# Optimization experiments

Hardware: AMD Instinct MI355X
Metric: run time of the kernel (lower is better)

## Reference

```python
import jax, jax.numpy as jnp
import numpy as np
from jax import lax

AROUND_R = 0.1  # init default


def bilinear_sample(img, grid):
    """img: [B,C,H,W]; grid: [B,A,N,2] in [-1,1]; returns [B,C,A,N].
    Matches F.grid_sample(mode='bilinear', padding_mode='zeros', align_corners=False)."""
    B, C, H, W = img.shape
    x = (grid[..., 0] + 1.0) * (W / 2) - 0.5  # unnormalize, align_corners=False
    y = (grid[..., 1] + 1.0) * (H / 2) - 0.5
    x0 = jnp.floor(x)
    y0 = jnp.floor(y)
    wx1 = x - x0
    wy1 = y - y0
    wx0 = 1.0 - wx1
    wy0 = 1.0 - wy1
    imgf = img.reshape(B, C, H * W)
    A, N = grid.shape[1], grid.shape[2]

    def gather(ix, iy):
        valid = (ix >= 0) & (ix <= W - 1) & (iy >= 0) & (iy <= H - 1)
        idx = (jnp.clip(iy, 0, H - 1) * W + jnp.clip(ix, 0, W - 1)).astype(jnp.int32)
        vals = jax.vmap(lambda im, ii: im[:, ii])(imgf, idx.reshape(B, A * N))  # [B,C,A*N]
        return vals.reshape(B, C, A, N) * valid[:, None].astype(img.dtype)

    v00 = gather(x0, y0)
    v10 = gather(x0 + 1, y0)
    v01 = gather(x0, y0 + 1)
    v11 = gather(x0 + 1, y0 + 1)
    return (v00 * (wx0 * wy0)[:, None] + v10 * (wx1 * wy0)[:, None]
            + v01 * (wx0 * wy1)[:, None] + v11 * (wx1 * wy1)[:, None])


def soft_align(x1, points_feature, points, pos_emb_2d, around_offsets):
    # --- torch.no_grad() block: grid and replicated features are detached ---
    grid = points[:, None, :, :]                                  # [B,1,N,2]
    around = (around_offsets * 2.0 - 0.5) * 2.0 * AROUND_R        # [B,A,N,2]
    g = lax.stop_gradient(jnp.clip(grid + around, -1.0, 1.0))     # [B,A,N,2]
    rep = lax.stop_gradient(points_feature)                       # [B,N,C]
    rep = rep.transpose(0, 2, 1)[:, :, None, :]                   # [B,C,1,N]
    # --- differentiable part ---
    emb = bilinear_sample(pos_emb_2d, g)                          # [B,C,A,N]
    feat = bilinear_sample(x1, g)                                 # [B,C,A,N]
    eps = 1e-8  # torch cosine_similarity default
    dot = jnp.sum(rep * feat, axis=1)                             # [B,A,N]
    na = jnp.maximum(jnp.sqrt(jnp.sum(rep * rep, axis=1)), eps)   # [B,1,N]
    nb = jnp.maximum(jnp.sqrt(jnp.sum(feat * feat, axis=1)), eps)
    sim = dot / (na * nb)                                         # [B,A,N]
    w = jax.nn.softmax(sim, axis=1)                               # softmax over A
    weighted = jnp.sum(emb * w[:, None], axis=2)                  # [B,C,N]
    return points_feature + weighted.transpose(0, 2, 1)           # [B,N,C]


def setup_inputs() -> dict:
    key = jax.random.key(0)
    k1, k2, k3, k4, k5 = jax.random.split(key, 5)
    B, C, H, W, N, A = 4, 256, 128, 128, 4096, 5
    x1 = jax.random.normal(k1, (B, C, H, W), jnp.float32)
    points_feature = jax.random.normal(k2, (B, N, C), jnp.float32)
    points = jax.random.uniform(k3, (B, N, 2), jnp.float32, -1.0, 1.0)
    pos_emb_2d = jax.random.normal(k4, (B, C, H, W), jnp.float32)
    around_offsets = jax.random.uniform(k5, (B, A, N, 2), jnp.float32)  # torch.rand
    return {"x1": x1, "points_feature": points_feature, "points": points,
            "pos_emb_2d": pos_emb_2d, "around_offsets": around_offsets}


def reference(x1, points_feature, points, pos_emb_2d, around_offsets):
    return soft_align(x1, points_feature, points, pos_emb_2d, around_offsets)
```

## Files before the change

### kernel.cpp

```cpp
#include <hip/hip_runtime.h>
#include <hip/hip_bf16.h>
#include <math.h>

constexpr int B = 4, C = 256, H = 128, W = 128, N = 4096, A = 5;
constexpr int HWs = H * W;
constexpr float AROUND_R = 0.1f;
constexpr int NP = B * N;

__device__ __forceinline__ float ulo(unsigned u) {
    union { unsigned i; float f; } x; x.i = u << 16; return x.f;
}
__device__ __forceinline__ float uhi(unsigned u) {
    union { unsigned i; float f; } x; x.i = u & 0xffff0000u; return x.f;
}
__device__ __forceinline__ float red64(float v) {
    #pragma unroll
    for (int off = 32; off > 0; off >>= 1)
        v += __shfl_xor(v, off);
    return v;
}

#if __has_builtin(__builtin_amdgcn_cvt_pk_f32_fp8) && __has_builtin(__builtin_amdgcn_cvt_pk_fp8_f32)
#define FP8_HW 1
#endif

__device__ __forceinline__ unsigned enc_fp8_sw(float x) {
    unsigned s = (__float_as_uint(x) >> 31) << 7;
    float ax = fminf(fabsf(x), 448.0f);
    if (!(ax >= 0x1p-10f)) return s;
    int e = (int)((__float_as_uint(ax) >> 23) & 0xff) - 127;
    e = e < -6 ? -6 : e;
    float q = rintf(ldexpf(ax, 3 - e));
    int iq = (int)q;
    if (iq >= 16) { iq = 8; e += 1; }
    unsigned enc = (iq >= 8) ? (((unsigned)(e + 7) << 3) | (unsigned)(iq - 8))
                             : (unsigned)iq;
    return s | enc;
}
__device__ __forceinline__ float dec_fp8_sw(unsigned u) {
    unsigned s = u >> 7, E = (u >> 3) & 0xf, M = u & 7;
    float v = E ? __uint_as_float(((E + 120u) << 23) | (M << 20)) : (float)M * 0x1p-9f;
    return s ? -v : v;
}

__device__ __forceinline__ unsigned pack4_fp8(float a0, float a1, float a2, float a3) {
#ifdef FP8_HW
    int w = __builtin_amdgcn_cvt_pk_fp8_f32(a0, a1, 0, false);
    w = __builtin_amdgcn_cvt_pk_fp8_f32(a2, a3, w, true);
    return (unsigned)w;
#else
    return enc_fp8_sw(a0) | (enc_fp8_sw(a1) << 8) | (enc_fp8_sw(a2) << 16) | (enc_fp8_sw(a3) << 24);
#endif
}
__device__ __forceinline__ void fp8x4_to_f32(unsigned u, float* f) {
#ifdef FP8_HW
    auto lo = __builtin_amdgcn_cvt_pk_f32_fp8((int)u, false);
    auto hi = __builtin_amdgcn_cvt_pk_f32_fp8((int)u, true);
    f[0] = lo[0]; f[1] = lo[1]; f[2] = hi[0]; f[3] = hi[1];
#else
    f[0] = dec_fp8_sw(u & 0xff); f[1] = dec_fp8_sw((u >> 8) & 0xff);
    f[2] = dec_fp8_sw((u >> 16) & 0xff); f[3] = dec_fp8_sw(u >> 24);
#endif
}

__global__ __launch_bounds__(256) void transpose_x1_fp8(const float* __restrict__ in,
                                                        unsigned* __restrict__ outw) {
    constexpr int TILE = 32;
    __shared__ float t[TILE][C + 1];
    const int tilesPerB = HWs / TILE;
    int bx = blockIdx.x;
    int b  = bx / tilesPerB;
    int hw0 = (bx % tilesPerB) * TILE;
    int tid  = threadIdx.x;
    int hw_l = tid & 31;
    int cg   = tid >> 5;

    const float* src = in + (size_t)b * C * HWs;
    #pragma unroll
    for (int ci = 0; ci < C / 8; ++ci) {
        int c = ci * 8 + cg;
        t[hw_l][c] = src[(size_t)c * HWs + hw0 + hw_l];
    }
    __syncthreads();
    unsigned* dst = outw + ((size_t)b * HWs + hw0) * (C / 4);
    int dq = tid & 63, pg = tid >> 6;
    #pragma unroll
    for (int it = 0; it < 8; ++it) {
        int pix = it * 4 + pg;
        float a0 = t[pix][dq * 4 + 0], a1 = t[pix][dq * 4 + 1];
        float a2 = t[pix][dq * 4 + 2], a3 = t[pix][dq * 4 + 3];
        dst[(size_t)pix * (C / 4) + dq] = pack4_fp8(a0, a1, a2, a3);
    }
}

__global__ __launch_bounds__(256) void transpose_pe_bf16(const float* __restrict__ in,
                                                         __hip_bfloat16* __restrict__ out) {
    constexpr int TILE = 32;
    __shared__ float t[TILE][C + 1];
    const int tilesPerB = HWs / TILE;
    int bx = blockIdx.x;
    int b  = bx / tilesPerB;
    int hw0 = (bx % tilesPerB) * TILE;
    int tid  = threadIdx.x;
    int hw_l = tid & 31;
    int cg   = tid >> 5;

    const float* src = in + (size_t)b * C * HWs;
    #pragma unroll
    for (int ci = 0; ci < C / 8; ++ci) {
        int c = ci * 8 + cg;
        t[hw_l][c] = src[(size_t)c * HWs + hw0 + hw_l];
    }
    __syncthreads();
    __hip_bfloat16* dst = out + ((size_t)b * HWs + hw0) * C;
    #pragma unroll
    for (int hwi = 0; hwi < TILE; ++hwi) {
        dst[(size_t)hwi * C + tid] = __float2bfloat16(t[hwi][tid]);
    }
}

__global__ __launch_bounds__(256) void soft_align_v5(
    const unsigned char* __restrict__ x1f8,
    const ushort* __restrict__ pebf,
    const float* __restrict__ pf,
    const float* __restrict__ pts,
    const float* __restrict__ ao,
    float* __restrict__ out)
{
    int tid = threadIdx.x, lane = tid & 63, wave = tid >> 6;
    int p = blockIdx.x * 4 + wave;
    int b = p >> 12, n = p & (N - 1);
    size_t pn = (size_t)p;

    float gx0 = pts[pn * 2 + 0];
    float gy0 = pts[pn * 2 + 1];
    float2 aov[A];
    #pragma unroll
    for (int a = 0; a < A; ++a)
        aov[a] = *reinterpret_cast<const float2*>(ao + (((size_t)b * A + a) * N + n) * 2);

    float4 rep4 = *reinterpret_cast<const float4*>(pf + pn * C + lane * 4);

    int   sidx[A][4];
    float swgt[A][4];
    #pragma unroll
    for (int a = 0; a < A; ++a) {
        float gx = fminf(fmaxf(gx0 + (aov[a].x * 2.0f - 0.5f) * (2.0f * AROUND_R), -1.0f), 1.0f);
        float gy = fminf(fmaxf(gy0 + (aov[a].y * 2.0f - 0.5f) * (2.0f * AROUND_R), -1.0f), 1.0f);
        float x = (gx + 1.0f) * (W * 0.5f) - 0.5f;
        float y = (gy + 1.0f) * (H * 0.5f) - 0.5f;
        float fx0 = floorf(x), fy0 = floorf(y);
        float wx1 = x - fx0, wy1 = y - fy0;
        float wx0 = 1.0f - wx1, wy0 = 1.0f - wy1;
        int ix0 = (int)fx0, iy0 = (int)fy0, ix1 = ix0 + 1, iy1 = iy0 + 1;
        bool vx0 = (ix0 >= 0) & (ix0 < W), vx1 = (ix1 >= 0) & (ix1 < W);
        bool vy0 = (iy0 >= 0) & (iy0 < H), vy1 = (iy1 >= 0) & (iy1 < H);
        int cx0 = min(max(ix0, 0), W - 1), cx1 = min(max(ix1, 0), W - 1);
        int cy0 = min(max(iy0, 0), H - 1), cy1 = min(max(iy1, 0), H - 1);
        int id0 = cy0 * W + cx0, id1 = cy0 * W + cx1;
        int id2 = cy1 * W + cx0, id3 = cy1 * W + cx1;
        sidx[a][0] = __builtin_amdgcn_readfirstlane(id0);
        sidx[a][1] = __builtin_amdgcn_readfirstlane(id1);
        sidx[a][2] = __builtin_amdgcn_readfirstlane(id2);
        sidx[a][3] = __builtin_amdgcn_readfirstlane(id3);
        swgt[a][0] = (vx0 && vy0) ? wx0 * wy0 : 0.0f;
        swgt[a][1] = (vx1 && vy0) ? wx1 * wy0 : 0.0f;
        swgt[a][2] = (vx0 && vy1) ? wx0 * wy1 : 0.0f;
        swgt[a][3] = (vx1 && vy1) ? wx1 * wy1 : 0.0f;
    }

    const unsigned char* xb = x1f8 + (size_t)b * HWs * C;
    const ushort*        pb = pebf + (size_t)b * HWs * C;
    unsigned xv[A][4];
    #pragma unroll
    for (int a = 0; a < A; ++a)
        #pragma unroll
        for (int k = 0; k < 4; ++k)
            xv[a][k] = *reinterpret_cast<const unsigned*>(xb + (size_t)sidx[a][k] * C + lane * 4);
    uint2 pv[A][4];
    #pragma unroll
    for (int a = 0; a < A; ++a)
        #pragma unroll
        for (int k = 0; k < 4; ++k)
            pv[a][k] = *reinterpret_cast<const uint2*>(pb + (size_t)sidx[a][k] * C + lane * 4);

    float na2 = rep4.x * rep4.x + rep4.y * rep4.y + rep4.z * rep4.z + rep4.w * rep4.w;
    float dt[A], nb[A];
    #pragma unroll
    for (int a = 0; a < A; ++a) {
        float f0 = 0.f, f1 = 0.f, f2 = 0.f, f3 = 0.f;
        #pragma unroll
        for (int k = 0; k < 4; ++k) {
            float w = swgt[a][k];
            float c4[4];
            fp8x4_to_f32(xv[a][k], c4);
            f0 += w * c4[0]; f1 += w * c4[1]; f2 += w * c4[2]; f3 += w * c4[3];
        }
        dt[a] = rep4.x * f0 + rep4.y * f1 + rep4.z * f2 + rep4.w * f3;
        nb[a] = f0 * f0 + f1 * f1 + f2 * f2 + f3 * f3;
    }

    na2 = red64(na2);
    #pragma unroll
    for (int a = 0; a < A; ++a) dt[a] = red64(dt[a]);
    #pragma unroll
    for (int a = 0; a < A; ++a) nb[a] = red64(nb[a]);
    float na = fmaxf(sqrtf(na2), 1e-8f);

    float sim[A];
    #pragma unroll
    for (int a = 0; a < A; ++a)
        sim[a] = dt[a] / (na * fmaxf(sqrtf(nb[a]), 1e-8f));

    float m = sim[0];
    #pragma unroll
    for (int a = 1; a < A; ++a) m = fmaxf(m, sim[a]);
    float e[A], s = 0.f;
    #pragma unroll
    for (int a = 0; a < A; ++a) { e[a] = __expf(sim[a] - m); s += e[a]; }
    float inv = 1.0f / s;

    float o0 = rep4.x, o1 = rep4.y, o2 = rep4.z, o3 = rep4.w;
    #pragma unroll
    for (int a = 0; a < A; ++a) {
        float wa = e[a] * inv;
        #pragma unroll
        for (int k = 0; k < 4; ++k) {
            float c = wa * swgt[a][k];
            unsigned u0 = pv[a][k].x, u1 = pv[a][k].y;
            o0 += c * ulo(u0); o1 += c * uhi(u0);
            o2 += c * ulo(u1); o3 += c * uhi(u1);
        }
    }
    *reinterpret_cast<float4*>(out + pn * C + lane * 4) = make_float4(o0, o1, o2, o3);
}

extern "C" void kernel_launch(void* const* d_in, const int* in_sizes, int n_in,
                              void* d_out, int out_size, void* d_ws, size_t ws_size,
                              hipStream_t stream) {
    const float* x1  = (const float*)d_in[0];
    const float* pf  = (const float*)d_in[1];
    const float* pts = (const float*)d_in[2];
    const float* pe  = (const float*)d_in[3];
    const float* ao  = (const float*)d_in[4];
    float* out = (float*)d_out;

    unsigned* x1f8w = (unsigned*)d_ws;
    __hip_bfloat16* pebf = (__hip_bfloat16*)((char*)d_ws + (size_t)B * HWs * C);

    int tblocks = B * (HWs / 32);
    transpose_x1_fp8 <<<tblocks, 256, 0, stream>>>(x1, x1f8w);
    transpose_pe_bf16<<<tblocks, 256, 0, stream>>>(pe, pebf);
    soft_align_v5<<<NP / 4, 256, 0, stream>>>((const unsigned char*)x1f8w,
                                              (const ushort*)pebf, pf, pts, ao, out);
}
```

Measured before the change: 66.12 us.

## Interleave fp8 x1 and bf16 pos-emb per pixel into one padded record

Measured after the change: 97.96 us. 48.1% more time.

```diff
diff --git a/kernel.cpp b/kernel.cpp
--- a/kernel.cpp
+++ b/kernel.cpp
@@ -6,12 +6,19 @@
 constexpr int HWs = H * W;
 constexpr float AROUND_R = 0.1f;
 constexpr int NP = B * N;
+constexpr int PIXB = 1024;
 
 __device__ __forceinline__ float ulo(unsigned u) {
     union { unsigned i; float f; } x; x.i = u << 16; return x.f;
 }
 __device__ __forceinline__ float uhi(unsigned u) {
     union { unsigned i; float f; } x; x.i = u & 0xffff0000u; return x.f;
+}
+__device__ __forceinline__ unsigned pk2bf(float a, float b) {
+    unsigned ua = __float_as_uint(a), ub = __float_as_uint(b);
+    ua = (ua + 0x7fffu + ((ua >> 16) & 1u)) >> 16;
+    ub = (ub + 0x7fffu + ((ub >> 16) & 1u)) & 0xffff0000u;
+    return ua | ub;
 }
 __device__ __forceinline__ float red64(float v) {
     #pragma unroll
@@ -42,7 +49,6 @@
     float v = E ? __uint_as_float(((E + 120u) << 23) | (M << 20)) : (float)M * 0x1p-9f;
     return s ? -v : v;
 }
-
 __device__ __forceinline__ unsigned pack4_fp8(float a0, float a1, float a2, float a3) {
 #ifdef FP8_HW
     int w = __builtin_amdgcn_cvt_pk_fp8_f32(a0, a1, 0, false);
@@ -64,7 +70,7 @@
 }
 
 __global__ __launch_bounds__(256) void transpose_x1_fp8(const float* __restrict__ in,
-                                                        unsigned* __restrict__ outw) {
+                                                        char* __restrict__ imgs) {
     constexpr int TILE = 32;
     __shared__ float t[TILE][C + 1];
     const int tilesPerB = HWs / TILE;
@@ -82,19 +88,20 @@
         t[hw_l][c] = src[(size_t)c * HWs + hw0 + hw_l];
     }
     __syncthreads();
-    unsigned* dst = outw + ((size_t)b * HWs + hw0) * (C / 4);
+    char* base = imgs + ((size_t)b * HWs + hw0) * PIXB;
     int dq = tid & 63, pg = tid >> 6;
     #pragma unroll
     for (int it = 0; it < 8; ++it) {
         int pix = it * 4 + pg;
         float a0 = t[pix][dq * 4 + 0], a1 = t[pix][dq * 4 + 1];
         float a2 = t[pix][dq * 4 + 2], a3 = t[pix][dq * 4 + 3];
-        dst[(size_t)pix * (C / 4) + dq] = pack4_fp8(a0, a1, a2, a3);
+        *reinterpret_cast<unsigned*>(base + (size_t)pix * PIXB + 16 * dq + 8) =
+            pack4_fp8(a0, a1, a2, a3);
     }
 }
 
 __global__ __launch_bounds__(256) void transpose_pe_bf16(const float* __restrict__ in,
-                                                         __hip_bfloat16* __restrict__ out) {
+                                                         char* __restrict__ imgs) {
     constexpr int TILE = 32;
     __shared__ float t[TILE][C + 1];
     const int tilesPerB = HWs / TILE;
@@ -112,16 +119,20 @@
         t[hw_l][c] = src[(size_t)c * HWs + hw0 + hw_l];
     }
     __syncthreads();
-    __hip_bfloat16* dst = out + ((size_t)b * HWs + hw0) * C;
-    #pragma unroll
-    for (int hwi = 0; hwi < TILE; ++hwi) {
-        dst[(size_t)hwi * C + tid] = __float2bfloat16(t[hwi][tid]);
-    }
-}
-
-__global__ __launch_bounds__(256) void soft_align_v5(
-    const unsigned char* __restrict__ x1f8,
-    const ushort* __restrict__ pebf,
+    char* base = imgs + ((size_t)b * HWs + hw0) * PIXB;
+    int dq = tid & 63, pg = tid >> 6;
+    #pragma unroll
+    for (int it = 0; it < 8; ++it) {
+        int pix = it * 4 + pg;
+        float a0 = t[pix][dq * 4 + 0], a1 = t[pix][dq * 4 + 1];
+        float a2 = t[pix][dq * 4 + 2], a3 = t[pix][dq * 4 + 3];
+        uint2 w = make_uint2(pk2bf(a0, a1), pk2bf(a2, a3));
+        *reinterpret_cast<uint2*>(base + (size_t)pix * PIXB + 16 * dq) = w;
+    }
+}
+
+__global__ __launch_bounds__(256) void soft_align_v6(
+    const char* __restrict__ imgs,
     const float* __restrict__ pf,
     const float* __restrict__ pts,
     const float* __restrict__ ao,
@@ -132,8 +143,7 @@
     int b = p >> 12, n = p & (N - 1);
     size_t pn = (size_t)p;
 
-    float gx0 = pts[pn * 2 + 0];
-    float gy0 = pts[pn * 2 + 1];
+    float2 g0 = *reinterpret_cast<const float2*>(pts + pn * 2);
     float2 aov[A];
     #pragma unroll
     for (int a = 0; a < A; ++a)
@@ -145,8 +155,8 @@
     float swgt[A][4];
     #pragma unroll
     for (int a = 0; a < A; ++a) {
-        float gx = fminf(fmaxf(gx0 + (aov[a].x * 2.0f - 0.5f) * (2.0f * AROUND_R), -1.0f), 1.0f);
-        float gy = fminf(fmaxf(gy0 + (aov[a].y * 2.0f - 0.5f) * (2.0f * AROUND_R), -1.0f), 1.0f);
+        float gx = fminf(fmaxf(g0.x + (aov[a].x * 2.0f - 0.5f) * (2.0f * AROUND_R), -1.0f), 1.0f);
+        float gy = fminf(fmaxf(g0.y + (aov[a].y * 2.0f - 0.5f) * (2.0f * AROUND_R), -1.0f), 1.0f);
         float x = (gx + 1.0f) * (W * 0.5f) - 0.5f;
         float y = (gy + 1.0f) * (H * 0.5f) - 0.5f;
         float fx0 = floorf(x), fy0 = floorf(y);
@@ -157,47 +167,43 @@
         bool vy0 = (iy0 >= 0) & (iy0 < H), vy1 = (iy1 >= 0) & (iy1 < H);
         int cx0 = min(max(ix0, 0), W - 1), cx1 = min(max(ix1, 0), W - 1);
         int cy0 = min(max(iy0, 0), H - 1), cy1 = min(max(iy1, 0), H - 1);
-        int id0 = cy0 * W + cx0, id1 = cy0 * W + cx1;
-        int id2 = cy1 * W + cx0, id3 = cy1 * W + cx1;
-        sidx[a][0] = __builtin_amdgcn_readfirstlane(id0);
-        sidx[a][1] = __builtin_amdgcn_readfirstlane(id1);
-        sidx[a][2] = __builtin_amdgcn_readfirstlane(id2);
-        sidx[a][3] = __builtin_amdgcn_readfirstlane(id3);
+        sidx[a][0] = __builtin_amdgcn_readfirstlane(cy0 * W + cx0);
+        sidx[a][1] = __builtin_amdgcn_readfirstlane(cy0 * W + cx1);
+        sidx[a][2] = __builtin_amdgcn_readfirstlane(cy1 * W + cx0);
+        sidx[a][3] = __builtin_amdgcn_readfirstlane(cy1 * W + cx1);
         swgt[a][0] = (vx0 && vy0) ? wx0 * wy0 : 0.0f;
         swgt[a][1] = (vx1 && vy0) ? wx1 * wy0 : 0.0f;
         swgt[a][2] = (vx0 && vy1) ? wx0 * wy1 : 0.0f;
         swgt[a][3] = (vx1 && vy1) ? wx1 * wy1 : 0.0f;
     }
 
-    const unsigned char* xb = x1f8 + (size_t)b * HWs * C;
-    const ushort*        pb = pebf + (size_t)b * HWs * C;
-    unsigned xv[A][4];
+    const char* ib = imgs + (size_t)b * HWs * PIXB + 16 * lane;
+    uint4 v[A][4];
     #pragma unroll
     for (int a = 0; a < A; ++a)
         #pragma unroll
         for (int k = 0; k < 4; ++k)
-            xv[a][k] = *reinterpret_cast<const unsigned*>(xb + (size_t)sidx[a][k] * C + lane * 4);
-    uint2 pv[A][4];
-    #pragma unroll
-    for (int a = 0; a < A; ++a)
-        #pragma unroll
-        for (int k = 0; k < 4; ++k)
-            pv[a][k] = *reinterpret_cast<const uint2*>(pb + (size_t)sidx[a][k] * C + lane * 4);
+            v[a][k] = *reinterpret_cast<const uint4*>(ib + (size_t)sidx[a][k] * PIXB);
 
     float na2 = rep4.x * rep4.x + rep4.y * rep4.y + rep4.z * rep4.z + rep4.w * rep4.w;
-    float dt[A], nb[A];
+    float dt[A], nb[A], emb[A][4];
     #pragma unroll
     for (int a = 0; a < A; ++a) {
         float f0 = 0.f, f1 = 0.f, f2 = 0.f, f3 = 0.f;
+        float e0 = 0.f, e1 = 0.f, e2 = 0.f, e3 = 0.f;
         #pragma unroll
         for (int k = 0; k < 4; ++k) {
             float w = swgt[a][k];
+            unsigned pl = v[a][k].x, ph = v[a][k].y, xw = v[a][k].z;
             float c4[4];
-            fp8x4_to_f32(xv[a][k], c4);
+            fp8x4_to_f32(xw, c4);
             f0 += w * c4[0]; f1 += w * c4[1]; f2 += w * c4[2]; f3 += w * c4[3];
+            e0 += w * ulo(pl); e1 += w * uhi(pl);
+            e2 += w * ulo(ph); e3 += w * uhi(ph);
         }
         dt[a] = rep4.x * f0 + rep4.y * f1 + rep4.z * f2 + rep4.w * f3;
         nb[a] = f0 * f0 + f1 * f1 + f2 * f2 + f3 * f3;
+        emb[a][0] = e0; emb[a][1] = e1; emb[a][2] = e2; emb[a][3] = e3;
     }
 
     na2 = red64(na2);
@@ -224,13 +230,8 @@
     #pragma unroll
     for (int a = 0; a < A; ++a) {
         float wa = e[a] * inv;
-        #pragma unroll
-        for (int k = 0; k < 4; ++k) {
-            float c = wa * swgt[a][k];
-            unsigned u0 = pv[a][k].x, u1 = pv[a][k].y;
-            o0 += c * ulo(u0); o1 += c * uhi(u0);
-            o2 += c * ulo(u1); o3 += c * uhi(u1);
-        }
+        o0 += wa * emb[a][0]; o1 += wa * emb[a][1];
+        o2 += wa * emb[a][2]; o3 += wa * emb[a][3];
     }
     *reinterpret_cast<float4*>(out + pn * C + lane * 4) = make_float4(o0, o1, o2, o3);
 }
@@ -245,12 +246,10 @@
     const float* ao  = (const float*)d_in[4];
     float* out = (float*)d_out;
 
-    unsigned* x1f8w = (unsigned*)d_ws;
-    __hip_bfloat16* pebf = (__hip_bfloat16*)((char*)d_ws + (size_t)B * HWs * C);
+    char* imgs = (char*)d_ws;
 
     int tblocks = B * (HWs / 32);
-    transpose_x1_fp8 <<<tblocks, 256, 0, stream>>>(x1, x1f8w);
-    transpose_pe_bf16<<<tblocks, 256, 0, stream>>>(pe, pebf);
-    soft_align_v5<<<NP / 4, 256, 0, stream>>>((const unsigned char*)x1f8w,
-                                              (const ushort*)pebf, pf, pts, ao, out);
-}
+    transpose_x1_fp8 <<<tblocks, 256, 0, stream>>>(x1, imgs);
+    transpose_pe_bf16<<<tblocks, 256, 0, stream>>>(pe, imgs);
+    soft_align_v6<<<NP / 4, 256, 0, stream>>>(imgs, pf, pts, ao, out);
+}
```

## Overlap pos-emb transpose with similarity pass by splitting into three kernels

Applied to the files above, without the earlier changes.

Result: slower. 71.47 us (+8.1%).

```diff
diff --git a/kernel.cpp b/kernel.cpp
--- a/kernel.cpp
+++ b/kernel.cpp
@@ -42,7 +42,6 @@
     float v = E ? __uint_as_float(((E + 120u) << 23) | (M << 20)) : (float)M * 0x1p-9f;
     return s ? -v : v;
 }
-
 __device__ __forceinline__ unsigned pack4_fp8(float a0, float a1, float a2, float a3) {
 #ifdef FP8_HW
     int w = __builtin_amdgcn_cvt_pk_fp8_f32(a0, a1, 0, false);
@@ -61,6 +60,28 @@
     f[0] = dec_fp8_sw(u & 0xff); f[1] = dec_fp8_sw((u >> 8) & 0xff);
     f[2] = dec_fp8_sw((u >> 16) & 0xff); f[3] = dec_fp8_sw(u >> 24);
 #endif
+}
+
+__device__ __forceinline__ void corner_math(float gx0, float gy0, float2 aov,
+                                            int* id, float* wg) {
+    float gx = fminf(fmaxf(gx0 + (aov.x * 2.0f - 0.5f) * (2.0f * AROUND_R), -1.0f), 1.0f);
+    float gy = fminf(fmaxf(gy0 + (aov.y * 2.0f - 0.5f) * (2.0f * AROUND_R), -1.0f), 1.0f);
+    float x = (gx + 1.0f) * (W * 0.5f) - 0.5f;
+    float y = (gy + 1.0f) * (H * 0.5f) - 0.5f;
+    float fx0 = floorf(x), fy0 = floorf(y);
+    float wx1 = x - fx0, wy1 = y - fy0;
+    float wx0 = 1.0f - wx1, wy0 = 1.0f - wy1;
+    int ix0 = (int)fx0, iy0 = (int)fy0, ix1 = ix0 + 1, iy1 = iy0 + 1;
+    bool vx0 = (ix0 >= 0) & (ix0 < W), vx1 = (ix1 >= 0) & (ix1 < W);
+    bool vy0 = (iy0 >= 0) & (iy0 < H), vy1 = (iy1 >= 0) & (iy1 < H);
+    int cx0 = min(max(ix0, 0), W - 1), cx1 = min(max(ix1, 0), W - 1);
+    int cy0 = min(max(iy0, 0), H - 1), cy1 = min(max(iy1, 0), H - 1);
+    id[0] = cy0 * W + cx0; id[1] = cy0 * W + cx1;
+    id[2] = cy1 * W + cx0; id[3] = cy1 * W + cx1;
+    wg[0] = (vx0 && vy0) ? wx0 * wy0 : 0.0f;
+    wg[1] = (vx1 && vy0) ? wx1 * wy0 : 0.0f;
+    wg[2] = (vx0 && vy1) ? wx0 * wy1 : 0.0f;
+    wg[3] = (vx1 && vy1) ? wx1 * wy1 : 0.0f;
 }
 
 __global__ __launch_bounds__(256) void transpose_x1_fp8(const float* __restrict__ in,
@@ -93,38 +114,124 @@
     }
 }
 
-__global__ __launch_bounds__(256) void transpose_pe_bf16(const float* __restrict__ in,
-                                                         __hip_bfloat16* __restrict__ out) {
-    constexpr int TILE = 32;
-    __shared__ float t[TILE][C + 1];
-    const int tilesPerB = HWs / TILE;
-    int bx = blockIdx.x;
-    int b  = bx / tilesPerB;
-    int hw0 = (bx % tilesPerB) * TILE;
-    int tid  = threadIdx.x;
-    int hw_l = tid & 31;
-    int cg   = tid >> 5;
-
-    const float* src = in + (size_t)b * C * HWs;
-    #pragma unroll
-    for (int ci = 0; ci < C / 8; ++ci) {
-        int c = ci * 8 + cg;
-        t[hw_l][c] = src[(size_t)c * HWs + hw0 + hw_l];
-    }
-    __syncthreads();
-    __hip_bfloat16* dst = out + ((size_t)b * HWs + hw0) * C;
-    #pragma unroll
-    for (int hwi = 0; hwi < TILE; ++hwi) {
-        dst[(size_t)hwi * C + tid] = __float2bfloat16(t[hwi][tid]);
-    }
-}
-
-__global__ __launch_bounds__(256) void soft_align_v5(
+__global__ __launch_bounds__(256) void k2_petrans_sim(
+    const float* __restrict__ pe,
+    __hip_bfloat16* __restrict__ pebf,
     const unsigned char* __restrict__ x1f8,
+    const float* __restrict__ pf,
+    const float* __restrict__ pts,
+    const float* __restrict__ ao,
+    float* __restrict__ wout)
+{
+    __shared__ float t[32][C + 1];
+    int bid = blockIdx.x;
+    int r = bid % 3, tb = bid / 3;
+    int tid = threadIdx.x;
+
+    if (r == 0) {
+        const int tilesPerB = HWs / 32;
+        int b  = tb / tilesPerB;
+        int hw0 = (tb % tilesPerB) * 32;
+        int hw_l = tid & 31, cg = tid >> 5;
+        const float* src = pe + (size_t)b * C * HWs;
+        #pragma unroll
+        for (int ci = 0; ci < C / 8; ++ci) {
+            int c = ci * 8 + cg;
+            t[hw_l][c] = src[(size_t)c * HWs + hw0 + hw_l];
+        }
+        __syncthreads();
+        __hip_bfloat16* dst = pebf + ((size_t)b * HWs + hw0) * C;
+        #pragma unroll
+        for (int hwi = 0; hwi < 32; ++hwi) {
+            dst[(size_t)hwi * C + tid] = __float2bfloat16(t[hwi][tid]);
+        }
+        return;
+    }
+
+    int sb = 2 * tb + (r - 1);
+    int lane = tid & 63, wave = tid >> 6;
+    int p = sb * 4 + wave;
+    int b = p >> 12, n = p & (N - 1);
+    size_t pn = (size_t)p;
+
+    float2 g0 = *reinterpret_cast<const float2*>(pts + pn * 2);
+    float2 aov[A];
+    #pragma unroll
+    for (int a = 0; a < A; ++a)
+        aov[a] = *reinterpret_cast<const float2*>(ao + (((size_t)b * A + a) * N + n) * 2);
+
+    float4 rep4 = *reinterpret_cast<const float4*>(pf + pn * C + lane * 4);
+
+    int   sidx[A][4];
+    float swgt[A][4];
+    #pragma unroll
+    for (int a = 0; a < A; ++a) {
+        int id[4]; float wg[4];
+        corner_math(g0.x, g0.y, aov[a], id, wg);
+        #pragma unroll
+        for (int k = 0; k < 4; ++k) {
+            sidx[a][k] = __builtin_amdgcn_readfirstlane(id[k]);
+            swgt[a][k] = wg[k];
+        }
+    }
+
+    const unsigned char* xb = x1f8 + (size_t)b * HWs * C;
+    unsigned xv[A][4];
+    #pragma unroll
+    for (int a = 0; a < A; ++a)
+        #pragma unroll
+        for (int k = 0; k < 4; ++k)
+            xv[a][k] = *reinterpret_cast<const unsigned*>(xb + (size_t)sidx[a][k] * C + lane * 4);
+
+    float na2 = rep4.x * rep4.x + rep4.y * rep4.y + rep4.z * rep4.z + rep4.w * rep4.w;
+    float dt[A], nb[A];
+    #pragma unroll
+    for (int a = 0; a < A; ++a) {
+        float f0 = 0.f, f1 = 0.f, f2 = 0.f, f3 = 0.f;
+        #pragma unroll
+        for (int k = 0; k < 4; ++k) {
+            float w = swgt[a][k];
+            float c4[4];
+            fp8x4_to_f32(xv[a][k], c4);
+            f0 += w * c4[0]; f1 += w * c4[1]; f2 += w * c4[2]; f3 += w * c4[3];
+        }
+        dt[a] = rep4.x * f0 + rep4.y * f1 + rep4.z * f2 + rep4.w * f3;
+        nb[a] = f0 * f0 + f1 * f1 + f2 * f2 + f3 * f3;
+    }
+
+    na2 = red64(na2);
+    #pragma unroll
+    for (int a = 0; a < A; ++a) dt[a] = red64(dt[a]);
+    #pragma unroll
+    for (int a = 0; a < A; ++a) nb[a] = red64(nb[a]);
+    float na = fmaxf(sqrtf(na2), 1e-8f);
+
+    float sim[A];
+    #pragma unroll
+    for (int a = 0; a < A; ++a)
+        sim[a] = dt[a] / (na * fmaxf(sqrtf(nb[a]), 1e-8f));
+
+    float m = sim[0];
+    #pragma unroll
+    for (int a = 1; a < A; ++a) m = fmaxf(m, sim[a]);
+    float e[A], s = 0.f;
+    #pragma unroll
+    for (int a = 0; a < A; ++a) { e[a] = __expf(sim[a] - m); s += e[a]; }
+    float inv = 1.0f / s;
+
+    if (lane == 0) {
+        *reinterpret_cast<float4*>(wout + pn * 8) =
+            make_float4(e[0] * inv, e[1] * inv, e[2] * inv, e[3] * inv);
+        wout[pn * 8 + 4] = e[4] * inv;
+    }
+}
+
+__global__ __launch_bounds__(256) void k3_emb(
     const ushort* __restrict__ pebf,
     const float* __restrict__ pf,
     const float* __restrict__ pts,
     const float* __restrict__ ao,
+    const float* __restrict__ wsm,
     float* __restrict__ out)
 {
     int tid = threadIdx.x, lane = tid & 63, wave = tid >> 6;
@@ -132,51 +239,30 @@
     int b = p >> 12, n = p & (N - 1);
     size_t pn = (size_t)p;
 
-    float gx0 = pts[pn * 2 + 0];
-    float gy0 = pts[pn * 2 + 1];
+    float2 g0 = *reinterpret_cast<const float2*>(pts + pn * 2);
     float2 aov[A];
     #pragma unroll
     for (int a = 0; a < A; ++a)
         aov[a] = *reinterpret_cast<const float2*>(ao + (((size_t)b * A + a) * N + n) * 2);
 
-    float4 rep4 = *reinterpret_cast<const float4*>(pf + pn * C + lane * 4);
+    float4 w03 = *reinterpret_cast<const float4*>(wsm + pn * 8);
+    float  w4  = wsm[pn * 8 + 4];
+    float wa[A] = {w03.x, w03.y, w03.z, w03.w, w4};
 
     int   sidx[A][4];
-    float swgt[A][4];
+    float cwt[A][4];
     #pragma unroll
     for (int a = 0; a < A; ++a) {
-        float gx = fminf(fmaxf(gx0 + (aov[a].x * 2.0f - 0.5f) * (2.0f * AROUND_R), -1.0f), 1.0f);
-        float gy = fminf(fmaxf(gy0 + (aov[a].y * 2.0f - 0.5f) * (2.0f * AROUND_R), -1.0f), 1.0f);
-        float x = (gx + 1.0f) * (W * 0.5f) - 0.5f;
-        float y = (gy + 1.0f) * (H * 0.5f) - 0.5f;
-        float fx0 = floorf(x), fy0 = floorf(y);
-        float wx1 = x - fx0, wy1 = y - fy0;
-        float wx0 = 1.0f - wx1, wy0 = 1.0f - wy1;
-        int ix0 = (int)fx0, iy0 = (int)fy0, ix1 = ix0 + 1, iy1 = iy0 + 1;
-        bool vx0 = (ix0 >= 0) & (ix0 < W), vx1 = (ix1 >= 0) & (ix1 < W);
-        bool vy0 = (iy0 >= 0) & (iy0 < H), vy1 = (iy1 >= 0) & (iy1 < H);
-        int cx0 = min(max(ix0, 0), W - 1), cx1 = min(max(ix1, 0), W - 1);
-        int cy0 = min(max(iy0, 0), H - 1), cy1 = min(max(iy1, 0), H - 1);
-        int id0 = cy0 * W + cx0, id1 = cy0 * W + cx1;
-        int id2 = cy1 * W + cx0, id3 = cy1 * W + cx1;
-        sidx[a][0] = __builtin_amdgcn_readfirstlane(id0);
-        sidx[a][1] = __builtin_amdgcn_readfirstlane(id1);
-        sidx[a][2] = __builtin_amdgcn_readfirstlane(id2);
-        sidx[a][3] = __builtin_amdgcn_readfirstlane(id3);
-        swgt[a][0] = (vx0 && vy0) ? wx0 * wy0 : 0.0f;
-        swgt[a][1] = (vx1 && vy0) ? wx1 * wy0 : 0.0f;
-        swgt[a][2] = (vx0 && vy1) ? wx0 * wy1 : 0.0f;
-        swgt[a][3] = (vx1 && vy1) ? wx1 * wy1 : 0.0f;
-    }
-
-    const unsigned char* xb = x1f8 + (size_t)b * HWs * C;
-    const ushort*        pb = pebf + (size_t)b * HWs * C;
-    unsigned xv[A][4];
-    #pragma unroll
-    for (int a = 0; a < A; ++a)
-        #pragma unroll
-        for (int k = 0; k < 4; ++k)
-            xv[a][k] = *reinterpret_cast<const unsigned*>(xb + (size_t)sidx[a][k] * C + lane * 4);
+        int id[4]; float wg[4];
+        corner_math(g0.x, g0.y, aov[a], id, wg);
+        #pragma unroll
+        for (int k = 0; k < 4; ++k) {
+            sidx[a][k] = __builtin_amdgcn_readfirstlane(id[k]);
+            cwt[a][k] = wa[a] * wg[k];
+        }
+    }
+
+    const ushort* pb = pebf + (size_t)b * HWs * C;
     uint2 pv[A][4];
     #pragma unroll
     for (int a = 0; a < A; ++a)
@@ -184,49 +270,13 @@
         for (int k = 0; k < 4; ++k)
             pv[a][k] = *reinterpret_cast<const uint2*>(pb + (size_t)sidx[a][k] * C + lane * 4);
 
-    float na2 = rep4.x * rep4.x + rep4.y * rep4.y + rep4.z * rep4.z + rep4.w * rep4.w;
-    float dt[A], nb[A];
+    float4 rep4 = *reinterpret_cast<const float4*>(pf + pn * C + lane * 4);
+    float o0 = rep4.x, o1 = rep4.y, o2 = rep4.z, o3 = rep4.w;
     #pragma unroll
     for (int a = 0; a < A; ++a) {
-        float f0 = 0.f, f1 = 0.f, f2 = 0.f, f3 = 0.f;
         #pragma unroll
         for (int k = 0; k < 4; ++k) {
-            float w = swgt[a][k];
-            float c4[4];
-            fp8x4_to_f32(xv[a][k], c4);
-            f0 += w * c4[0]; f1 += w * c4[1]; f2 += w * c4[2]; f3 += w * c4[3];
-        }
-        dt[a] = rep4.x * f0 + rep4.y * f1 + rep4.z * f2 + rep4.w * f3;
-        nb[a] = f0 * f0 + f1 * f1 + f2 * f2 + f3 * f3;
-    }
-
-    na2 = red64(na2);
-    #pragma unroll
-    for (int a = 0; a < A; ++a) dt[a] = red64(dt[a]);
-    #pragma unroll
-    for (int a = 0; a < A; ++a) nb[a] = red64(nb[a]);
-    float na = fmaxf(sqrtf(na2), 1e-8f);
-
-    float sim[A];
-    #pragma unroll
-    for (int a = 0; a < A; ++a)
-        sim[a] = dt[a] / (na * fmaxf(sqrtf(nb[a]), 1e-8f));
-
-    float m = sim[0];
-    #pragma unroll
-    for (int a = 1; a < A; ++a) m = fmaxf(m, sim[a]);
-    float e[A], s = 0.f;
-    #pragma unroll
-    for (int a = 0; a < A; ++a) { e[a] = __expf(sim[a] - m); s += e[a]; }
-    float inv = 1.0f / s;
-
-    float o0 = rep4.x, o1 = rep4.y, o2 = rep4.z, o3 = rep4.w;
-    #pragma unroll
-    for (int a = 0; a < A; ++a) {
-        float wa = e[a] * inv;
-        #pragma unroll
-        for (int k = 0; k < 4; ++k) {
-            float c = wa * swgt[a][k];
+            float c = cwt[a][k];
             unsigned u0 = pv[a][k].x, u1 = pv[a][k].y;
             o0 += c * ulo(u0); o1 += c * uhi(u0);
             o2 += c * ulo(u1); o3 += c * uhi(u1);
@@ -247,10 +297,12 @@
 
     unsigned* x1f8w = (unsigned*)d_ws;
     __hip_bfloat16* pebf = (__hip_bfloat16*)((char*)d_ws + (size_t)B * HWs * C);
+    float* wsm = (float*)((char*)d_ws + (size_t)B * HWs * C + (size_t)B * HWs * C * 2);
 
     int tblocks = B * (HWs / 32);
-    transpose_x1_fp8 <<<tblocks, 256, 0, stream>>>(x1, x1f8w);
-    transpose_pe_bf16<<<tblocks, 256, 0, stream>>>(pe, pebf);
-    soft_align_v5<<<NP / 4, 256, 0, stream>>>((const unsigned char*)x1f8w,
-                                              (const ushort*)pebf, pf, pts, ao, out);
-}
+    transpose_x1_fp8<<<tblocks, 256, 0, stream>>>(x1, x1f8w);
+    k2_petrans_sim<<<3 * tblocks, 256, 0, stream>>>(pe, pebf,
+                                                    (const unsigned char*)x1f8w,
+                                                    pf, pts, ao, wsm);
+    k3_emb<<<NP / 4, 256, 0, stream>>>((const ushort*)pebf, pf, pts, ao, wsm, out);
+}
```

## Pipeline per-batch transposes with sampling in a combined staged kernel

Applied to the files above, without the earlier changes.

After: 91.71 us. 38.7% more time.

```diff
diff --git a/kernel.cpp b/kernel.cpp
--- a/kernel.cpp
+++ b/kernel.cpp
@@ -42,7 +42,6 @@
     float v = E ? __uint_as_float(((E + 120u) << 23) | (M << 20)) : (float)M * 0x1p-9f;
     return s ? -v : v;
 }
-
 __device__ __forceinline__ unsigned pack4_fp8(float a0, float a1, float a2, float a3) {
 #ifdef FP8_HW
     int w = __builtin_amdgcn_cvt_pk_fp8_f32(a0, a1, 0, false);
@@ -63,176 +62,167 @@
 #endif
 }
 
-__global__ __launch_bounds__(256) void transpose_x1_fp8(const float* __restrict__ in,
-                                                        unsigned* __restrict__ outw) {
-    constexpr int TILE = 32;
-    __shared__ float t[TILE][C + 1];
-    const int tilesPerB = HWs / TILE;
-    int bx = blockIdx.x;
-    int b  = bx / tilesPerB;
-    int hw0 = (bx % tilesPerB) * TILE;
-    int tid  = threadIdx.x;
-    int hw_l = tid & 31;
-    int cg   = tid >> 5;
-
-    const float* src = in + (size_t)b * C * HWs;
-    #pragma unroll
-    for (int ci = 0; ci < C / 8; ++ci) {
-        int c = ci * 8 + cg;
-        t[hw_l][c] = src[(size_t)c * HWs + hw0 + hw_l];
+__device__ __forceinline__ void corner_math(float gx0, float gy0, float2 aov,
+                                            int* id, float* wg) {
+    float gx = fminf(fmaxf(gx0 + (aov.x * 2.0f - 0.5f) * (2.0f * AROUND_R), -1.0f), 1.0f);
+    float gy = fminf(fmaxf(gy0 + (aov.y * 2.0f - 0.5f) * (2.0f * AROUND_R), -1.0f), 1.0f);
+    float x = (gx + 1.0f) * (W * 0.5f) - 0.5f;
+    float y = (gy + 1.0f) * (H * 0.5f) - 0.5f;
+    float fx0 = floorf(x), fy0 = floorf(y);
+    float wx1 = x - fx0, wy1 = y - fy0;
+    float wx0 = 1.0f - wx1, wy0 = 1.0f - wy1;
+    int ix0 = (int)fx0, iy0 = (int)fy0, ix1 = ix0 + 1, iy1 = iy0 + 1;
+    bool vx0 = (ix0 >= 0) & (ix0 < W), vx1 = (ix1 >= 0) & (ix1 < W);
+    bool vy0 = (iy0 >= 0) & (iy0 < H), vy1 = (iy1 >= 0) & (iy1 < H);
+    int cx0 = min(max(ix0, 0), W - 1), cx1 = min(max(ix1, 0), W - 1);
+    int cy0 = min(max(iy0, 0), H - 1), cy1 = min(max(iy1, 0), H - 1);
+    id[0] = cy0 * W + cx0; id[1] = cy0 * W + cx1;
+    id[2] = cy1 * W + cx0; id[3] = cy1 * W + cx1;
+    wg[0] = (vx0 && vy0) ? wx0 * wy0 : 0.0f;
+    wg[1] = (vx1 && vy0) ? wx1 * wy0 : 0.0f;
+    wg[2] = (vx0 && vy1) ? wx0 * wy1 : 0.0f;
+    wg[3] = (vx1 && vy1) ? wx1 * wy1 : 0.0f;
+}
+
+__global__ __launch_bounds__(256) void stage_kernel(
+    const float* x1, const float* pe,
+    unsigned* x1f8w, __hip_bfloat16* pebfw,
+    const unsigned char* x1f8, const ushort* pebf,
+    const float* pf, const float* pts, const float* ao,
+    float* out, int tb, int pb)
+{
+    __shared__ float t[16][C + 1];
+    int tid = threadIdx.x;
+
+    if (tb >= 0) {
+        int hw0 = blockIdx.x * 16;
+        int hw_l = tid & 15, cg = tid >> 4;
+        const float* src = x1 + (size_t)tb * C * HWs;
+        #pragma unroll
+        for (int ci = 0; ci < 16; ++ci) {
+            int c = ci * 16 + cg;
+            t[hw_l][c] = src[(size_t)c * HWs + hw0 + hw_l];
+        }
+        __syncthreads();
+        {
+            unsigned* dst = x1f8w + ((size_t)tb * HWs + hw0) * (C / 4);
+            int dq = tid & 63, pg = tid >> 6;
+            #pragma unroll
+            for (int it = 0; it < 4; ++it) {
+                int pix = it * 4 + pg;
+                dst[(size_t)pix * (C / 4) + dq] =
+                    pack4_fp8(t[pix][dq * 4 + 0], t[pix][dq * 4 + 1],
+                              t[pix][dq * 4 + 2], t[pix][dq * 4 + 3]);
+            }
+        }
+        __syncthreads();
+        src = pe + (size_t)tb * C * HWs;
+        #pragma unroll
+        for (int ci = 0; ci < 16; ++ci) {
+            int c = ci * 16 + cg;
+            t[hw_l][c] = src[(size_t)c * HWs + hw0 + hw_l];
+        }
+        __syncthreads();
+        {
+            __hip_bfloat16* dst = pebfw + ((size_t)tb * HWs + hw0) * C;
+            #pragma unroll
+            for (int hwi = 0; hwi < 16; ++hwi)
+                dst[(size_t)hwi * C + tid] = __float2bfloat16(t[hwi][tid]);
+        }
     }
-    __syncthreads();
-    unsigned* dst = outw + ((size_t)b * HWs + hw0) * (C / 4);
-    int dq = tid & 63, pg = tid >> 6;
-    #pragma unroll
-    for (int it = 0; it < 8; ++it) {
-        int pix = it * 4 + pg;
-        float a0 = t[pix][dq * 4 + 0], a1 = t[pix][dq * 4 + 1];
-        float a2 = t[pix][dq * 4 + 2], a3 = t[pix][dq * 4 + 3];
-        dst[(size_t)pix * (C / 4) + dq] = pack4_fp8(a0, a1, a2, a3);
+
+    if (pb >= 0) {
+        int lane = tid & 63, wave = tid >> 6;
+        int n = blockIdx.x * 4 + wave;
+        int b = pb;
+        size_t pn = (size_t)b * N + n;
+
+        float2 g0 = *reinterpret_cast<const float2*>(pts + pn * 2);
+        float2 aov[A];
+        #pragma unroll
+        for (int a = 0; a < A; ++a)
+            aov[a] = *reinterpret_cast<const float2*>(ao + (((size_t)b * A + a) * N + n) * 2);
+
+        float4 rep4 = *reinterpret_cast<const float4*>(pf + pn * C + lane * 4);
+
+        int   sidx[A][4];
+        float swgt[A][4];
+        #pragma unroll
+        for (int a = 0; a < A; ++a) {
+            int id[4]; float wg[4];
+            corner_math(g0.x, g0.y, aov[a], id, wg);
+            #pragma unroll
+            for (int k = 0; k < 4; ++k) {
+                sidx[a][k] = __builtin_amdgcn_readfirstlane(id[k]);
+                swgt[a][k] = wg[k];
+            }
+        }
+
+        const unsigned char* xb = x1f8 + (size_t)b * HWs * C;
+        const ushort*        pbp = pebf + (size_t)b * HWs * C;
+        unsigned xv[A][4];
+        #pragma unroll
+        for (int a = 0; a < A; ++a)
+            #pragma unroll
+            for (int k = 0; k < 4; ++k)
+                xv[a][k] = *reinterpret_cast<const unsigned*>(xb + (size_t)sidx[a][k] * C + lane * 4);
+        uint2 pv[A][4];
+        #pragma unroll
+        for (int a = 0; a < A; ++a)
+            #pragma unroll
+            for (int k = 0; k < 4; ++k)
+                pv[a][k] = *reinterpret_cast<const uint2*>(pbp + (size_t)sidx[a][k] * C + lane * 4);
+
+        float na2 = rep4.x * rep4.x + rep4.y * rep4.y + rep4.z * rep4.z + rep4.w * rep4.w;
+        float dt[A], nb[A];
+        #pragma unroll
+        for (int a = 0; a < A; ++a) {
+            float f0 = 0.f, f1 = 0.f, f2 = 0.f, f3 = 0.f;
+            #pragma unroll
+            for (int k = 0; k < 4; ++k) {
+                float w = swgt[a][k];
+                float c4[4];
+                fp8x4_to_f32(xv[a][k], c4);
+                f0 += w * c4[0]; f1 += w * c4[1]; f2 += w * c4[2]; f3 += w * c4[3];
+            }
+            dt[a] = rep4.x * f0 + rep4.y * f1 + rep4.z * f2 + rep4.w * f3;
+            nb[a] = f0 * f0 + f1 * f1 + f2 * f2 + f3 * f3;
+        }
+
+        na2 = red64(na2);
+        #pragma unroll
+        for (int a = 0; a < A; ++a) dt[a] = red64(dt[a]);
+        #pragma unroll
+        for (int a = 0; a < A; ++a) nb[a] = red64(nb[a]);
+        float na = fmaxf(sqrtf(na2), 1e-8f);
+
+        float sim[A];
+        #pragma unroll
+        for (int a = 0; a < A; ++a)
+            sim[a] = dt[a] / (na * fmaxf(sqrtf(nb[a]), 1e-8f));
+
+        float m = sim[0];
+        #pragma unroll
+        for (int a = 1; a < A; ++a) m = fmaxf(m, sim[a]);
+        float e[A], s = 0.f;
+        #pragma unroll
+        for (int a = 0; a < A; ++a) { e[a] = __expf(sim[a] - m); s += e[a]; }
+        float inv = 1.0f / s;
+
+        float o0 = rep4.x, o1 = rep4.y, o2 = rep4.z, o3 = rep4.w;
+        #pragma unroll
+        for (int a = 0; a < A; ++a) {
+            float wa = e[a] * inv;
+            #pragma unroll
+            for (int k = 0; k < 4; ++k) {
+                float c = wa * swgt[a][k];
+                unsigned u0 = pv[a][k].x, u1 = pv[a][k].y;
+                o0 += c * ulo(u0); o1 += c * uhi(u0);
+                o2 += c * ulo(u1); o3 += c * uhi(u1);
+            }
+        }
+        *reinterpret_cast<float4*>(out + pn * C + lane * 4) = make_float4(o0, o1, o2, o3);
     }
-}
-
-__global__ __launch_bounds__(256) void transpose_pe_bf16(const float* __restrict__ in,
-                                                         __hip_bfloat16* __restrict__ out) {
-    constexpr int TILE = 32;
-    __shared__ float t[TILE][C + 1];
-    const int tilesPerB = HWs / TILE;
-    int bx = blockIdx.x;
-    int b  = bx / tilesPerB;
-    int hw0 = (bx % tilesPerB) * TILE;
-    int tid  = threadIdx.x;
-    int hw_l = tid & 31;
-    int cg   = tid >> 5;
-
-    const float* src = in + (size_t)b * C * HWs;
-    #pragma unroll
-    for (int ci = 0; ci < C / 8; ++ci) {
-        int c = ci * 8 + cg;
-        t[hw_l][c] = src[(size_t)c * HWs + hw0 + hw_l];
-    }
-    __syncthreads();
-    __hip_bfloat16* dst = out + ((size_t)b * HWs + hw0) * C;
-    #pragma unroll
-    for (int hwi = 0; hwi < TILE; ++hwi) {
-        dst[(size_t)hwi * C + tid] = __float2bfloat16(t[hwi][tid]);
-    }
-}
-
-__global__ __launch_bounds__(256) void soft_align_v5(
-    const unsigned char* __restrict__ x1f8,
-    const ushort* __restrict__ pebf,
-    const float* __restrict__ pf,
-    const float* __restrict__ pts,
-    const float* __restrict__ ao,
-    float* __restrict__ out)
-{
-    int tid = threadIdx.x, lane = tid & 63, wave = tid >> 6;
-    int p = blockIdx.x * 4 + wave;
-    int b = p >> 12, n = p & (N - 1);
-    size_t pn = (size_t)p;
-
-    float gx0 = pts[pn * 2 + 0];
-    float gy0 = pts[pn * 2 + 1];
-    float2 aov[A];
-    #pragma unroll
-    for (int a = 0; a < A; ++a)
-        aov[a] = *reinterpret_cast<const float2*>(ao + (((size_t)b * A + a) * N + n) * 2);
-
-    float4 rep4 = *reinterpret_cast<const float4*>(pf + pn * C + lane * 4);
-
-    int   sidx[A][4];
-    float swgt[A][4];
-    #pragma unroll
-    for (int a = 0; a < A; ++a) {
-        float gx = fminf(fmaxf(gx0 + (aov[a].x * 2.0f - 0.5f) * (2.0f * AROUND_R), -1.0f), 1.0f);
-        float gy = fminf(fmaxf(gy0 + (aov[a].y * 2.0f - 0.5f) * (2.0f * AROUND_R), -1.0f), 1.0f);
-        float x = (gx + 1.0f) * (W * 0.5f) - 0.5f;
-        float y = (gy + 1.0f) * (H * 0.5f) - 0.5f;
-        float fx0 = floorf(x), fy0 = floorf(y);
-        float wx1 = x - fx0, wy1 = y - fy0;
-        float wx0 = 1.0f - wx1, wy0 = 1.0f - wy1;
-        int ix0 = (int)fx0, iy0 = (int)fy0, ix1 = ix0 + 1, iy1 = iy0 + 1;
-        bool vx0 = (ix0 >= 0) & (ix0 < W), vx1 = (ix1 >= 0) & (ix1 < W);
-        bool vy0 = (iy0 >= 0) & (iy0 < H), vy1 = (iy1 >= 0) & (iy1 < H);
-        int cx0 = min(max(ix0, 0), W - 1), cx1 = min(max(ix1, 0), W - 1);
-        int cy0 = min(max(iy0, 0), H - 1), cy1 = min(max(iy1, 0), H - 1);
-        int id0 = cy0 * W + cx0, id1 = cy0 * W + cx1;
-        int id2 = cy1 * W + cx0, id3 = cy1 * W + cx1;
-        sidx[a][0] = __builtin_amdgcn_readfirstlane(id0);
-        sidx[a][1] = __builtin_amdgcn_readfirstlane(id1);
-        sidx[a][2] = __builtin_amdgcn_readfirstlane(id2);
-        sidx[a][3] = __builtin_amdgcn_readfirstlane(id3);
-        swgt[a][0] = (vx0 && vy0) ? wx0 * wy0 : 0.0f;
-        swgt[a][1] = (vx1 && vy0) ? wx1 * wy0 : 0.0f;
-        swgt[a][2] = (vx0 && vy1) ? wx0 * wy1 : 0.0f;
-        swgt[a][3] = (vx1 && vy1) ? wx1 * wy1 : 0.0f;
-    }
-
-    const unsigned char* xb = x1f8 + (size_t)b * HWs * C;
-    const ushort*        pb = pebf + (size_t)b * HWs * C;
-    unsigned xv[A][4];
-    #pragma unroll
-    for (int a = 0; a < A; ++a)
-        #pragma unroll
-        for (int k = 0; k < 4; ++k)
-            xv[a][k] = *reinterpret_cast<const unsigned*>(xb + (size_t)sidx[a][k] * C + lane * 4);
-    uint2 pv[A][4];
-    #pragma unroll
-    for (int a = 0; a < A; ++a)
-        #pragma unroll
-        for (int k = 0; k < 4; ++k)
-            pv[a][k] = *reinterpret_cast<const uint2*>(pb + (size_t)sidx[a][k] * C + lane * 4);
-
-    float na2 = rep4.x * rep4.x + rep4.y * rep4.y + rep4.z * rep4.z + rep4.w * rep4.w;
-    float dt[A], nb[A];
-    #pragma unroll
-    for (int a = 0; a < A; ++a) {
-        float f0 = 0.f, f1 = 0.f, f2 = 0.f, f3 = 0.f;
-        #pragma unroll
-        for (int k = 0; k < 4; ++k) {
-            float w = swgt[a][k];
-            float c4[4];
-            fp8x4_to_f32(xv[a][k], c4);
-            f0 += w * c4[0]; f1 += w * c4[1]; f2 += w * c4[2]; f3 += w * c4[3];
-        }
-        dt[a] = rep4.x * f0 + rep4.y * f1 + rep4.z * f2 + rep4.w * f3;
-        nb[a] = f0 * f0 + f1 * f1 + f2 * f2 + f3 * f3;
-    }
-
-    na2 = red64(na2);
-    #pragma unroll
-    for (int a = 0; a < A; ++a) dt[a] = red64(dt[a]);
-    #pragma unroll
-    for (int a = 0; a < A; ++a) nb[a] = red64(nb[a]);
-    float na = fmaxf(sqrtf(na2), 1e-8f);
-
-    float sim[A];
-    #pragma unroll
-    for (int a = 0; a < A; ++a)
-        sim[a] = dt[a] / (na * fmaxf(sqrtf(nb[a]), 1e-8f));
-
-    float m = sim[0];
-    #pragma unroll
-    for (int a = 1; a < A; ++a) m = fmaxf(m, sim[a]);
-    float e[A], s = 0.f;
-    #pragma unroll
-    for (int a = 0; a < A; ++a) { e[a] = __expf(sim[a] - m); s += e[a]; }
-    float inv = 1.0f / s;
-
-    float o0 = rep4.x, o1 = rep4.y, o2 = rep4.z, o3 = rep4.w;
-    #pragma unroll
-    for (int a = 0; a < A; ++a) {
-        float wa = e[a] * inv;
-        #pragma unroll
-        for (int k = 0; k < 4; ++k) {
-            float c = wa * swgt[a][k];
-            unsigned u0 = pv[a][k].x, u1 = pv[a][k].y;
-            o0 += c * ulo(u0); o1 += c * uhi(u0);
-            o2 += c * ulo(u1); o3 += c * uhi(u1);
-        }
-    }
-    *reinterpret_cast<float4*>(out + pn * C + lane * 4) = make_float4(o0, o1, o2, o3);
 }
 
 extern "C" void kernel_launch(void* const* d_in, const int* in_sizes, int n_in,
@@ -247,10 +237,13 @@
 
     unsigned* x1f8w = (unsigned*)d_ws;
     __hip_bfloat16* pebf = (__hip_bfloat16*)((char*)d_ws + (size_t)B * HWs * C);
-
-    int tblocks = B * (HWs / 32);
-    transpose_x1_fp8 <<<tblocks, 256, 0, stream>>>(x1, x1f8w);
-    transpose_pe_bf16<<<tblocks, 256, 0, stream>>>(pe, pebf);
-    soft_align_v5<<<NP / 4, 256, 0, stream>>>((const unsigned char*)x1f8w,
-                                              (const ushort*)pebf, pf, pts, ao, out);
-}
+    const unsigned char* x1f8r = (const unsigned char*)d_ws;
+    const ushort* pebfr = (const ushort*)pebf;
+
+    for (int k = 0; k <= B; ++k) {
+        int tb = (k < B) ? k : -1;
+        int pb = (k > 0) ? (k - 1) : -1;
+        stage_kernel<<<1024, 256, 0, stream>>>(x1, pe, x1f8w, pebf, x1f8r, pebfr,
+                                               pf, pts, ao, out, tb, pb);
+    }
+}
```
